# Performance work log

Hardware: AMD Instinct MI355X
Metric: run time of the kernel (lower is better)

The kernel has to match this reference:

```python
import jax, jax.numpy as jnp
import numpy as np

K = 20        # neighbors kept per sample (module default k=20)
LAM = 50.0    # loss weight (module default lam=50)
EPS = 1e-6    # torch pairwise_distance eps, added inside |.|
CHUNK = 128   # row-chunk size for the O(N^2 C) L1 distance


def setup_inputs() -> dict:
    key = jax.random.key(0)
    k1, k2, k3 = jax.random.split(key, 3)
    N, C, NCLS = 2048, 256, 8
    return {
        "feature": jax.random.normal(k1, (N, C), jnp.float32),
        "scores": jax.random.normal(k2, (N, NCLS), jnp.float32),
        "target": jax.random.randint(k3, (N,), 0, NCLS),
    }


def reference(feature, scores, target):
    N, C = feature.shape
    # F.cross_entropy with default mean reduction
    logp = jax.nn.log_softmax(scores, axis=-1)
    ce = -jnp.mean(jnp.take_along_axis(logp, target[:, None], axis=1))

    # Pairwise eps-shifted L1 distances: D[i,j] = sum_c |x_i,c - x_j,c + eps|
    # (torch pairwise_distance on (C,1) views, summed). Chunked over rows to
    # avoid materializing an [N,N,C] tensor.
    def chunk_dist(xc):  # xc: [CHUNK, C] -> [CHUNK, N]
        return jnp.sum(jnp.abs(xc[:, None, :] - feature[None, :, :] + EPS), axis=-1)

    D = jax.lax.map(chunk_dist, feature.reshape(N // CHUNK, CHUNK, C)).reshape(N, N)

    # Same-label mask excluding self; invalid pairs pushed to +inf so top_k
    # of -D never selects them ahead of valid neighbors.
    same = (target[:, None] == target[None, :]) & (~jnp.eye(N, dtype=bool))
    Dm = jnp.where(same, D, jnp.inf)
    counts = jnp.sum(same, axis=1)          # same-label candidates per row
    m = jnp.minimum(counts, K)              # len(nums) in the original code

    _, idx = jax.lax.top_k(-Dm, K)          # indices of K smallest distances
    valid = jnp.arange(K)[None, :] < m[:, None]

    m_safe = jnp.maximum(m, 1).astype(feature.dtype)
    neigh = feature[idx]                    # [N, K, C]
    # mse_loss(feature[i], feature[j]/m, size_average=False) = sum over C
    diff = feature[:, None, :] - neigh / m_safe[:, None, None]
    per = jnp.sum(diff * diff, axis=-1)     # [N, K]
    per = jnp.where(valid, per, 0.0)
    return ce + LAM * 0.5 * jnp.sum(per)
```

## Files before the change

### kernel.cpp

```cpp
#include <hip/hip_runtime.h>
#include <math.h>


constexpr float EPS      = 1e-6f;
constexpr int   KSEL     = 20;
constexpr float LAM_HALF = 25.0f;
constexpr int   NCLS     = 8;

#define MAXC 512
#define LDP  68

__device__ __forceinline__ float finf() { return __builtin_inff(); }


__global__ __launch_bounds__(256) void setup_kernel(const int* __restrict__ T,
                                                    int N, int* __restrict__ meta) {
    __shared__ int cnt[256 * NCLS];
    __shared__ int cstart[NCLS + 1];
    const int tid = threadIdx.x;
    const int per = N / 256;

    int lc[NCLS];
    int myT[16];
#pragma unroll
    for (int c = 0; c < NCLS; ++c) lc[c] = 0;
    for (int q = 0; q < per; ++q) {
        int t = T[tid * per + q];
        myT[q] = t;
        ++lc[t];
    }
#pragma unroll
    for (int c = 0; c < NCLS; ++c) cnt[tid * NCLS + c] = lc[c];
    __syncthreads();

    if (tid < NCLS) {
        int off = 0;
        for (int t = 0; t < 256; ++t) {
            int v = cnt[t * NCLS + tid];
            cnt[t * NCLS + tid] = off;
            off += v;
        }
        cstart[tid] = off;
    }
    __syncthreads();
    if (tid == 0) {
        int tot[NCLS], acc = 0;
        for (int c = 0; c < NCLS; ++c) tot[c] = cstart[c];
        for (int c = 0; c < NCLS; ++c) { cstart[c] = acc; acc += tot[c]; }
        cstart[NCLS] = acc;
        for (int c = 0; c <= NCLS; ++c) meta[N + c] = cstart[c];
        int nt = 0;
        for (int c = 0; c < NCLS; ++c) {
            int nb = (tot[c] + 63) >> 6;
            for (int bi = 0; bi < nb; ++bi)
                for (int bj = bi; bj < nb; ++bj)
                    meta[N + 32 + nt++] = (c << 16) | (bi << 8) | bj;
        }
        meta[N + 16] = nt;
    }
    __syncthreads();

    int rc[NCLS];
#pragma unroll
    for (int c = 0; c < NCLS; ++c) rc[c] = 0;
    for (int q = 0; q < per; ++q) {
        int t = myT[q];
        int pos = cstart[t] + cnt[tid * NCLS + t] + rc[t]++;
        meta[pos] = tid * per + q;
    }
}

__global__ __launch_bounds__(256) void dist_kernel(const float* __restrict__ F,
                                                   const int* __restrict__ meta,
                                                   float* __restrict__ Dc,
                                                   int N, int C) {
    const int nt = meta[N + 16];
    const int t  = blockIdx.x >> 1;
    if (t >= nt) return;
    const int kh = blockIdx.x & 1;
    const int e    = meta[N + 32 + t];
    const int c    = e >> 16, bi = (e >> 8) & 255, bj = e & 255;
    const int base = meta[N + c];
    const int ncls = meta[N + c + 1] - base;
    const int i0 = bi * 64, j0 = bj * 64;
    const bool mirror = (bi != bj);
    float* __restrict__ Dh = Dc + (size_t)kh * N * MAXC;

    __shared__ float As[64 * LDP];
    __shared__ float Bs[64 * LDP];
    __shared__ int gi[64], gj[64];

    const int tid = threadIdx.x;
    const int tx = tid & 15, ty = tid >> 4;

    if (tid < 64)       gi[tid]      = meta[base + min(i0 + tid, ncls - 1)];
    else if (tid < 128) gj[tid - 64] = meta[base + min(j0 + (tid - 64), ncls - 1)];
    __syncthreads();

    float acc[4][4];
#pragma unroll
    for (int r = 0; r < 4; ++r)
#pragma unroll
        for (int s = 0; s < 4; ++s) acc[r][s] = 0.f;

    const int ck0 = kh * (C / 2);
    for (int ck = ck0; ck < ck0 + C / 2; ck += 64) {
#pragma unroll
        for (int it = 0; it < 4; ++it) {
            int slot = tid + it * 256;
            int row  = slot >> 4;
            int c4   = (slot & 15) << 2;
            float4 av = *(const float4*)&F[(size_t)gi[row] * C + ck + c4];
            av.x += EPS; av.y += EPS; av.z += EPS; av.w += EPS;
            *(float4*)&As[row * LDP + c4] = av;
            *(float4*)&Bs[row * LDP + c4] =
                *(const float4*)&F[(size_t)gj[row] * C + ck + c4];
        }
        __syncthreads();
#pragma unroll 4
        for (int c4 = 0; c4 < 64; c4 += 4) {
            float4 a[4], b[4];
#pragma unroll
            for (int r = 0; r < 4; ++r) a[r] = *(const float4*)&As[(ty * 4 + r) * LDP + c4];
#pragma unroll
            for (int s = 0; s < 4; ++s) b[s] = *(const float4*)&Bs[(tx + 16 * s) * LDP + c4];
#pragma unroll
            for (int r = 0; r < 4; ++r)
#pragma unroll
                for (int s = 0; s < 4; ++s) {
                    acc[r][s] += (fabsf(a[r].x - b[s].x) + fabsf(a[r].y - b[s].y))
                               + (fabsf(a[r].z - b[s].z) + fabsf(a[r].w - b[s].w));
                }
        }
        __syncthreads();
    }

#pragma unroll
    for (int r = 0; r < 4; ++r) {
        const int il = i0 + ty * 4 + r;
        if (il >= ncls) continue;
#pragma unroll
        for (int s = 0; s < 4; ++s) {
            const int jl = j0 + tx + 16 * s;
            if (jl >= ncls) continue;
            float val = (il != jl) ? acc[r][s] : finf();
            Dh[(size_t)(base + il) * MAXC + jl] = val;
            if (mirror) Dh[(size_t)(base + jl) * MAXC + il] = val;
        }
    }
}

__global__ __launch_bounds__(64) void select_kernel(const float* __restrict__ F,
                                                    const float* __restrict__ Dc,
                                                    const int* __restrict__ meta,
                                                    float* __restrict__ P,
                                                    int N, int C) {
    __shared__ int ssel[KSEL];
    const int s    = blockIdx.x;
    const int lane = threadIdx.x;

    int c = 0;
#pragma unroll
    for (int q = 1; q <= NCLS; ++q) c += (s >= meta[N + q]) ? 1 : 0;
    const int base = meta[N + c];
    const int ncls = meta[N + c + 1] - base;
    const float4* drow0 = (const float4*)(Dc + (size_t)s * MAXC);
    const float4* drow1 = (const float4*)(Dc + (size_t)(N + s) * MAXC);

    float v[8];
#pragma unroll
    for (int q = 0; q < 2; ++q) {
        float4 t0 = drow0[q * 64 + lane];
        float4 t1 = drow1[q * 64 + lane];
        int col = q * 256 + 4 * lane;
        v[q * 4 + 0] = (col + 0 < ncls) ? (t0.x + t1.x) : finf();
        v[q * 4 + 1] = (col + 1 < ncls) ? (t0.y + t1.y) : finf();
        v[q * 4 + 2] = (col + 2 < ncls) ? (t0.z + t1.z) : finf();
        v[q * 4 + 3] = (col + 3 < ncls) ? (t0.w + t1.w) : finf();
    }

    const int m = min(ncls - 1, KSEL);

    float lmin = finf();
#pragma unroll
    for (int i = 0; i < 8; ++i) lmin = fminf(lmin, v[i]);

    int mx = 0;
    for (int k = 0; k < m; ++k) {
        float w = lmin;
#pragma unroll
        for (int o = 1; o < 64; o <<= 1) w = fminf(w, __shfl_xor(w, o, 64));
        if (!(w < 1e37f)) break;
        unsigned long long mask = __ballot(lmin == w);
        int winner = (int)__builtin_ctzll(mask);
        if (lane == winner) {
            bool found = false;
            int  jl = 0;
#pragma unroll
            for (int i = 0; i < 8; ++i) {
                bool hit = !found && (v[i] == w);
                if (hit) { jl = (i >> 2) * 256 + 4 * lane + (i & 3); v[i] = finf(); found = true; }
            }
            ssel[k] = jl;
            float nm = finf();
#pragma unroll
            for (int i = 0; i < 8; ++i) nm = fminf(nm, v[i]);
            lmin = nm;
        }
        ++mx;
    }
    __syncthreads();

    float total = 0.f;
    if (mx > 0) {
        const float inv = 1.f / (float)m;
        const int   gi  = meta[s];
        float4 fi = ((const float4*)(F + (size_t)gi * C))[lane];
        float acc = 0.f;
        for (int k = 0; k < mx; ++k) {
            const int gj = meta[base + ssel[k]];
            float4 fj = ((const float4*)(F + (size_t)gj * C))[lane];
            float dx = fi.x - fj.x * inv;
            float dy = fi.y - fj.y * inv;
            float dz = fi.z - fj.z * inv;
            float dw = fi.w - fj.w * inv;
            acc += (dx * dx + dy * dy) + (dz * dz + dw * dw);
        }
        for (int o = 32; o > 0; o >>= 1) acc += __shfl_down(acc, o, 64);
        total = LAM_HALF * acc;
    }
    if (lane == 0) P[s] = total;
}

__global__ __launch_bounds__(256) void finalize_kernel(const float* __restrict__ scores,
                                                       const int* __restrict__ target,
                                                       const float* __restrict__ P,
                                                       float* __restrict__ out,
                                                       int N, int NC) {
    int tid = threadIdx.x;
    float ce = 0.f, dg = 0.f;
    for (int r = tid; r < N; r += 256) {
        const float* sc = scores + (size_t)r * NC;
        float mx = -3.4e38f;
        for (int c = 0; c < NC; ++c) mx = fmaxf(mx, sc[c]);
        float sum = 0.f;
        for (int c = 0; c < NC; ++c) sum += __expf(sc[c] - mx);
        ce += mx + __logf(sum) - sc[target[r]];
        dg += P[r];
    }
    __shared__ float redc[4], redd[4];
    for (int o = 32; o > 0; o >>= 1) { ce += __shfl_down(ce, o, 64); dg += __shfl_down(dg, o, 64); }
    int wid = tid >> 6, lane = tid & 63;
    if (lane == 0) { redc[wid] = ce; redd[wid] = dg; }
    __syncthreads();
    if (tid == 0)
        out[0] = (redc[0] + redc[1] + redc[2] + redc[3]) / (float)N
               + (redd[0] + redd[1] + redd[2] + redd[3]);
}

extern "C" void kernel_launch(void* const* d_in, const int* in_sizes, int n_in,
                              void* d_out, int out_size, void* d_ws, size_t ws_size,
                              hipStream_t stream) {
    const float* feature = (const float*)d_in[0];
    const float* scores  = (const float*)d_in[1];
    const int*   target  = (const int*)d_in[2];
    const int N  = in_sizes[2];
    const int C  = in_sizes[0] / N;
    const int NC = in_sizes[1] / N;
    float* out = (float*)d_out;

    float* Dc   = (float*)d_ws;
    int*   meta = (int*)((char*)d_ws + (size_t)2 * N * MAXC * sizeof(float));
    float* P    = (float*)((char*)d_ws + (size_t)2 * N * MAXC * sizeof(float) + 16384);

    setup_kernel<<<1, 256, 0, stream>>>(target, N, meta);

    const int NB = N / 64;
    const int max_tiles = NB * (NB + 1) / 2;
    dist_kernel<<<max_tiles * 2, 256, 0, stream>>>(feature, meta, Dc, N, C);

    select_kernel<<<N, 64, 0, stream>>>(feature, Dc, meta, P, N, C);

    finalize_kernel<<<1, 256, 0, stream>>>(scores, target, P, out, N, NC);
}
```

Baseline: 121.4 us.

## Fold finalize into dist and select kernels; parallelize setup prefix scan

Result: slower. 147.9 us (+21.9%).

```diff
diff --git a/kernel.cpp b/kernel.cpp
--- a/kernel.cpp
+++ b/kernel.cpp
@@ -33,14 +33,21 @@
     for (int c = 0; c < NCLS; ++c) cnt[tid * NCLS + c] = lc[c];
     __syncthreads();
 
-    if (tid < NCLS) {
-        int off = 0;
-        for (int t = 0; t < 256; ++t) {
-            int v = cnt[t * NCLS + tid];
-            cnt[t * NCLS + tid] = off;
-            off += v;
-        }
-        cstart[tid] = off;
+    {
+        const int g = tid >> 5, l = tid & 31;
+        int carry = 0;
+        for (int q = 0; q < 256; q += 32) {
+            int v = cnt[(q + l) * NCLS + g];
+            int x = v;
+#pragma unroll
+            for (int o = 1; o < 32; o <<= 1) {
+                int y = __shfl_up(x, o, 32);
+                if (l >= o) x += y;
+            }
+            cnt[(q + l) * NCLS + g] = carry + (x - v);
+            carry += __shfl(x, 31, 32);
+        }
+        if (l == 31) cstart[g] = carry;
     }
     __syncthreads();
     if (tid == 0) {
@@ -57,6 +64,7 @@
                     meta[N + 32 + nt++] = (c << 16) | (bi << 8) | bj;
         }
         meta[N + 16] = nt;
+        meta[N + 17] = 0;
     }
     __syncthreads();
 
@@ -73,7 +81,31 @@
 __global__ __launch_bounds__(256) void dist_kernel(const float* __restrict__ F,
                                                    const int* __restrict__ meta,
                                                    float* __restrict__ Dc,
-                                                   int N, int C) {
+                                                   const float* __restrict__ scores,
+                                                   const int* __restrict__ target,
+                                                   float* __restrict__ P,
+                                                   int N, int C, int NC) {
+    if (blockIdx.x == gridDim.x - 1) {
+        const int tid = threadIdx.x;
+        float ce = 0.f;
+        for (int r = tid; r < N; r += 256) {
+            const float* sc = scores + (size_t)r * NC;
+            float mx = -3.4e38f;
+            for (int c = 0; c < NC; ++c) mx = fmaxf(mx, sc[c]);
+            float sum = 0.f;
+            for (int c = 0; c < NC; ++c) sum += __expf(sc[c] - mx);
+            ce += mx + __logf(sum) - sc[target[r]];
+        }
+        __shared__ float redc[4];
+        for (int o = 32; o > 0; o >>= 1) ce += __shfl_down(ce, o, 64);
+        int wid = tid >> 6, lane = tid & 63;
+        if (lane == 0) redc[wid] = ce;
+        __syncthreads();
+        if (tid == 0)
+            P[N] = (redc[0] + redc[1] + redc[2] + redc[3]) / (float)N;
+        return;
+    }
+
     const int nt = meta[N + 16];
     const int t  = blockIdx.x >> 1;
     if (t >= nt) return;
@@ -152,8 +184,9 @@
 
 __global__ __launch_bounds__(64) void select_kernel(const float* __restrict__ F,
                                                     const float* __restrict__ Dc,
-                                                    const int* __restrict__ meta,
+                                                    int* __restrict__ meta,
                                                     float* __restrict__ P,
+                                                    float* __restrict__ out,
                                                     int N, int C) {
     __shared__ int ssel[KSEL];
     const int s    = blockIdx.x;
@@ -230,32 +263,21 @@
         total = LAM_HALF * acc;
     }
     if (lane == 0) P[s] = total;
-}
-
-__global__ __launch_bounds__(256) void finalize_kernel(const float* __restrict__ scores,
-                                                       const int* __restrict__ target,
-                                                       const float* __restrict__ P,
-                                                       float* __restrict__ out,
-                                                       int N, int NC) {
-    int tid = threadIdx.x;
-    float ce = 0.f, dg = 0.f;
-    for (int r = tid; r < N; r += 256) {
-        const float* sc = scores + (size_t)r * NC;
-        float mx = -3.4e38f;
-        for (int c = 0; c < NC; ++c) mx = fmaxf(mx, sc[c]);
-        float sum = 0.f;
-        for (int c = 0; c < NC; ++c) sum += __expf(sc[c] - mx);
-        ce += mx + __logf(sum) - sc[target[r]];
-        dg += P[r];
-    }
-    __shared__ float redc[4], redd[4];
-    for (int o = 32; o > 0; o >>= 1) { ce += __shfl_down(ce, o, 64); dg += __shfl_down(dg, o, 64); }
-    int wid = tid >> 6, lane = tid & 63;
-    if (lane == 0) { redc[wid] = ce; redd[wid] = dg; }
-    __syncthreads();
-    if (tid == 0)
-        out[0] = (redc[0] + redc[1] + redc[2] + redc[3]) / (float)N
-               + (redd[0] + redd[1] + redd[2] + redd[3]);
+
+    int last = 0;
+    if (lane == 0) {
+        __threadfence();
+        unsigned old = atomicAdd((unsigned*)&meta[N + 17], 1u);
+        last = (old == (unsigned)(gridDim.x - 1)) ? 1 : 0;
+    }
+    last = __shfl(last, 0, 64);
+    if (last) {
+        __threadfence();
+        float acc2 = 0.f;
+        for (int r = lane; r < N; r += 64) acc2 += P[r];
+        for (int o = 32; o > 0; o >>= 1) acc2 += __shfl_down(acc2, o, 64);
+        if (lane == 0) out[0] = acc2 + P[N];
+    }
 }
 
 extern "C" void kernel_launch(void* const* d_in, const int* in_sizes, int n_in,
@@ -277,9 +299,8 @@
 
     const int NB = N / 64;
     const int max_tiles = NB * (NB + 1) / 2;
-    dist_kernel<<<max_tiles * 2, 256, 0, stream>>>(feature, meta, Dc, N, C);
-
-    select_kernel<<<N, 64, 0, stream>>>(feature, Dc, meta, P, N, C);
-
-    finalize_kernel<<<1, 256, 0, stream>>>(scores, target, P, out, N, NC);
+    dist_kernel<<<max_tiles * 2 + 1, 256, 0, stream>>>(feature, meta, Dc,
+                                                       scores, target, P, N, C, NC);
+
+    select_kernel<<<N, 64, 0, stream>>>(feature, Dc, meta, P, out, N, C);
 }
```
